# Optimization experiments

Measured on AMD Instinct MI355X. Metric: run time of the kernel, lower is better.

Reference implementation:

```python
import jax, jax.numpy as jnp
import numpy as np
import math

B, S, D, H = 4, 1024, 1024, 16
DK = D // H


def setup_inputs() -> dict:
    key = jax.random.key(0)
    ks = jax.random.split(key, 13)
    s = 1.0 / math.sqrt(D)
    inp = {
        "query": jax.random.normal(ks[0], (B, S, D), jnp.float32),
        "key": jax.random.normal(ks[1], (B, S, D), jnp.float32),
        "value": jax.random.normal(ks[2], (B, S, D), jnp.float32),
        "mask": jax.random.randint(ks[3], (B, S, S), 0, 2, jnp.int32),
        "wq": jax.random.normal(ks[4], (D, D), jnp.float32) * s,
        "bq": jax.random.normal(ks[5], (D,), jnp.float32) * s,
        "wk": jax.random.normal(ks[6], (D, D), jnp.float32) * s,
        "bk": jax.random.normal(ks[7], (D,), jnp.float32) * s,
        "wv": jax.random.normal(ks[8], (D, D), jnp.float32) * s,
        "bv": jax.random.normal(ks[9], (D,), jnp.float32) * s,
        "wo": jax.random.normal(ks[10], (D, D), jnp.float32) * s,
        "bo": jax.random.normal(ks[11], (D,), jnp.float32) * s,
    }
    return inp


def reference(query, key, value, mask, wq, bq, wk, bk, wv, bv, wo, bo):
    # QKV projections, split into heads: [B,S,D] -> [B,H,S,DK]
    def proj(x, w, b):
        return (x @ w.T + b).reshape(B, S, H, DK).transpose(0, 2, 1, 3)

    q = proj(query, wq, bq)
    k = proj(key, wk, bk)
    v = proj(value, wv, bv)

    scores = jnp.einsum("bhqd,bhkd->bhqk", q, k) / math.sqrt(DK)
    scores = scores + mask[:, None, :, :].astype(scores.dtype) * (-1e9)
    p = jax.nn.softmax(scores, axis=-1)
    x = jnp.einsum("bhqk,bhkd->bhqd", p, v)
    x = x.transpose(0, 2, 1, 3).reshape(B, S, D)
    # output projection (dropout is identity in eval)
    return x @ wo.T + bo
```

## Files before the change

### kernel.cpp

```cpp
#include <hip/hip_runtime.h>
#include <hip/hip_bf16.h>


typedef __bf16 bf16x8 __attribute__((ext_vector_type(8)));
typedef float f32x4 __attribute__((ext_vector_type(4)));
typedef unsigned short us8 __attribute__((ext_vector_type(8)));
typedef unsigned short us4 __attribute__((ext_vector_type(4)));

#define MFMA(a, b, c) __builtin_amdgcn_mfma_f32_16x16x32_bf16(a, b, c, 0, 0, 0)
#define EXP2(x) __builtin_amdgcn_exp2f(x)

__device__ __forceinline__ unsigned short f2b(float f) {
  return __builtin_bit_cast(unsigned short, __float2bfloat16(f));
}
__device__ __forceinline__ float b2f(unsigned short u) {
  return __builtin_bit_cast(float, (unsigned)u << 16);
}
__device__ __forceinline__ bf16x8 ldbf8(const unsigned short* p) {
  return __builtin_bit_cast(bf16x8, *reinterpret_cast<const us8*>(p));
}
__device__ __forceinline__ us8 cvt8(float4 a, float4 b) {
  us8 o;
  o[0] = f2b(a.x); o[1] = f2b(a.y); o[2] = f2b(a.z); o[3] = f2b(a.w);
  o[4] = f2b(b.x); o[5] = f2b(b.y); o[6] = f2b(b.z); o[7] = f2b(b.w);
  return o;
}
__device__ __forceinline__ void glds16(const void* g, void* l) {
  __builtin_amdgcn_global_load_lds(
      (const __attribute__((address_space(1))) unsigned int*)g,
      (__attribute__((address_space(3))) unsigned int*)l, 16, 0, 0);
}

__global__ __launch_bounds__(256)
void prep(const int* __restrict__ mask, const float* __restrict__ wq,
          const float* __restrict__ wk, const float* __restrict__ wv,
          unsigned short* __restrict__ Mf, unsigned short* __restrict__ Wb) {
  const int bid = blockIdx.x, tid = threadIdx.x;
  if (bid < 4096) {
    const int idx = bid * 256 + tid;
    const int wl = idx & 63, tile = idx >> 6;
    const int kt = tile & 63, qt = (tile >> 6) & 63, b = tile >> 12;
    const int lr = wl & 15, lg = wl >> 4;
    const int4 mv = *reinterpret_cast<const int4*>(
        mask + (size_t)(b * 1024 + qt * 16 + lr) * 1024 + kt * 16 + lg * 4);
    us4 o;
    o[0] = mv.x ? 0xCEACu : 0u;
    o[1] = mv.y ? 0xCEACu : 0u;
    o[2] = mv.z ? 0xCEACu : 0u;
    o[3] = mv.w ? 0xCEACu : 0u;
    *reinterpret_cast<us4*>(Mf + (size_t)idx * 4) = o;
  } else {
    const int b2 = bid - 4096;
    const int widx = b2 >> 9;
    const float* src = (widx == 0) ? wq : (widx == 1) ? wk : wv;
    const size_t off = (size_t)(b2 & 511) * 2048 + tid * 8;
    const float4* p = reinterpret_cast<const float4*>(src + off);
    *reinterpret_cast<us8*>(Wb + (size_t)widx * 1048576 + off) = cvt8(p[0], p[1]);
  }
}

__global__ __launch_bounds__(256)
void cvt_w(const float* __restrict__ src, unsigned short* __restrict__ dst) {
  const size_t off = (size_t)blockIdx.x * 2048 + threadIdx.x * 8;
  const float4* p = reinterpret_cast<const float4*>(src + off);
  *reinterpret_cast<us8*>(dst + off) = cvt8(p[0], p[1]);
}

#define GEMM_COMPUTE_HALF(buf, h2)                                             \
  {                                                                            \
    bf16x8 af[4], bfr[2];                                                      \
    _Pragma("unroll") for (int m = 0; m < 4; ++m) {                            \
      const int row = wr * 64 + m * 16 + lr;                                   \
      af[m] = ldbf8((const unsigned short*)((char*)&As[buf][0] + row * 128 +   \
                                            (((h2) * 64 + lg * 16) ^ swzc)));  \
    }                                                                          \
    _Pragma("unroll") for (int n = 0; n < 2; ++n) {                            \
      const int row = wc * 32 + n * 16 + lr;                                   \
      bfr[n] = ldbf8((const unsigned short*)((char*)&Bs[buf][0] + row * 128 +  \
                                             (((h2) * 64 + lg * 16) ^ swzc))); \
    }                                                                          \
    _Pragma("unroll") for (int m = 0; m < 4; ++m)                              \
        _Pragma("unroll") for (int n = 0; n < 2; ++n)                          \
        acc[m][n] = MFMA(af[m], bfr[n], acc[m][n]);                            \
  }

#define STA(buf, it, v)                                                        \
  *reinterpret_cast<us8*>((char*)&As[buf][0] + (srow + (it) * 32) * 128 +      \
                          (scolb ^ (((srow + (it) * 32) & 7) << 4))) = (v)

__global__ __launch_bounds__(256)
void gemm_qkv(const float* __restrict__ Aq, const float* __restrict__ Akk,
              const float* __restrict__ Av, const unsigned short* __restrict__ Wb,
              const float* __restrict__ bq, const float* __restrict__ bk,
              const float* __restrict__ bv, unsigned short* __restrict__ Qb,
              unsigned short* __restrict__ Kf, unsigned short* __restrict__ Vf,
              float qscale) {
  constexpr int K = 1024, N = 1024;
  __shared__ __align__(16) unsigned short As[2][128 * 64];
  __shared__ __align__(16) unsigned short Bs[2][64 * 64];
  const int lid = blockIdx.x + (blockIdx.y << 5) + (blockIdx.z << 9);
  const int xcd = lid & 7, slot = lid >> 3;
  const int chunk = ((slot >> 5) << 3) + xcd;
  const int pos = slot & 31;
  const int z = chunk >> 4;
  const int bm = (((chunk & 15) << 1) + (pos >> 4)) * 128;
  const int bn = (pos & 15) * 64;

  const float* A = (z == 0) ? Aq : (z == 1) ? Akk : Av;
  const unsigned short* Bw = Wb + (size_t)z * 1048576;
  const float* bias = (z == 0) ? bq : (z == 1) ? bk : bv;
  const int t = threadIdx.x;
  const int w = t >> 6, lane = t & 63, lr = lane & 15, lg = lane >> 4;
  const int wr = w >> 1, wc = w & 1;
  const int srow = t >> 3, scolb = (t & 7) * 16, scole = (t & 7) * 8;
  const int swzc = (lr & 7) << 4;

  f32x4 acc[4][2];
#pragma unroll
  for (int m = 0; m < 4; ++m)
#pragma unroll
    for (int n = 0; n < 2; ++n) acc[m][n] = f32x4{0.f, 0.f, 0.f, 0.f};

  auto stageB = [&](int k0, int buf) {
#pragma unroll
    for (int it = 0; it < 2; ++it) {
      const int s = it * 256 + t, row = s >> 3, cb = (s & 7) * 16;
      const char* g = (const char*)Bw + ((size_t)(bn + row) * 1024 + k0) * 2 +
                      (cb ^ ((row & 7) << 4));
      char* l = (char*)&Bs[buf][0] + (it * 256 + w * 64) * 16;
      glds16(g, l);
    }
  };

  {
#pragma unroll
    for (int it = 0; it < 4; ++it) {
      const float4* p =
          reinterpret_cast<const float4*>(A + (size_t)(bm + srow + it * 32) * K + scole);
      STA(0, it, cvt8(p[0], p[1]));
    }
    stageB(0, 0);
  }
  __syncthreads();

  for (int c = 0; c < 16; ++c) {
    const int buf = c & 1;
    float4 fa[8];
    if (c < 15) {
      const int k1 = (c + 1) * 64;
#pragma unroll
      for (int it = 0; it < 4; ++it) {
        const float4* p = reinterpret_cast<const float4*>(
            A + (size_t)(bm + srow + it * 32) * K + k1 + scole);
        fa[2 * it] = p[0];
        fa[2 * it + 1] = p[1];
      }
      stageB(k1, buf ^ 1);
    }
    GEMM_COMPUTE_HALF(buf, 0)
    GEMM_COMPUTE_HALF(buf, 1)
    if (c < 15) {
#pragma unroll
      for (int it = 0; it < 4; ++it) STA(buf ^ 1, it, cvt8(fa[2 * it], fa[2 * it + 1]));
    }
    __syncthreads();
  }

#pragma unroll
  for (int m = 0; m < 4; ++m) {
    const int mr = bm + wr * 64 + m * 16 + lg * 4;
#pragma unroll
    for (int nt = 0; nt < 2; ++nt) {
      const int n = bn + wc * 32 + nt * 16 + lr;
      const float bb = bias[n];
      if (z == 0) {
#pragma unroll
        for (int r = 0; r < 4; ++r)
          Qb[(size_t)(mr + r) * N + n] = f2b((acc[m][nt][r] + bb) * qscale);
      } else if (z == 1) {
        const int b2 = mr >> 10, s0 = mr & 1023, hh = n >> 6, dd = n & 63;
        const size_t base = (size_t)(b2 * 16 + hh) * 65536 + (size_t)(dd >> 5) * 32768 +
                            (size_t)(s0 >> 4) * 512 +
                            (size_t)((s0 & 15) | (((dd >> 3) & 3) << 4)) * 8 + (dd & 7);
#pragma unroll
        for (int r = 0; r < 4; ++r) Kf[base + r * 8] = f2b(acc[m][nt][r] + bb);
      } else {
        const int b2 = mr >> 10, s0 = mr & 1023, hh = n >> 6, dd = n & 63;
        const size_t base = (size_t)(b2 * 16 + hh) * 65536 + (size_t)(s0 >> 5) * 2048 +
                            (size_t)(dd >> 4) * 512 +
                            (size_t)((dd & 15) | (((s0 >> 3) & 3) << 4)) * 8 + (s0 & 7);
        us4 pk;
#pragma unroll
        for (int r = 0; r < 4; ++r) pk[r] = f2b(acc[m][nt][r] + bb);
        *reinterpret_cast<us4*>(&Vf[base]) = pk;
      }
    }
  }
}

__global__ __launch_bounds__(256)
void gemm_out(const unsigned short* __restrict__ A, const unsigned short* __restrict__ Bw,
              const float* __restrict__ bias, float* __restrict__ Out) {
  constexpr int K = 1024, N = 1024;
  __shared__ __align__(16) unsigned short As[2][128 * 64];
  __shared__ __align__(16) unsigned short Bs[2][64 * 64];
  const int lid = blockIdx.x + (blockIdx.y << 5);
  const int xcd = lid & 7, slot = lid >> 3;
  const int chunk = ((slot >> 5) << 3) + xcd;
  const int pos = slot & 31;
  const int bm = ((chunk << 1) + (pos >> 4)) * 128;
  const int bn = (pos & 15) * 64;
  const int t = threadIdx.x;
  const int w = t >> 6, lane = t & 63, lr = lane & 15, lg = lane >> 4;
  const int wr = w >> 1, wc = w & 1;
  const int swzc = (lr & 7) << 4;

  f32x4 acc[4][2];
#pragma unroll
  for (int m = 0; m < 4; ++m)
#pragma unroll
    for (int n = 0; n < 2; ++n) acc[m][n] = f32x4{0.f, 0.f, 0.f, 0.f};

  auto stageA = [&](int k0, int buf) {
#pragma unroll
    for (int it = 0; it < 4; ++it) {
      const int s = it * 256 + t, row = s >> 3, cb = (s & 7) * 16;
      const char* g = (const char*)A + ((size_t)(bm + row) * 1024 + k0) * 2 +
                      (cb ^ ((row & 7) << 4));
      char* l = (char*)&As[buf][0] + (it * 256 + w * 64) * 16;
      glds16(g, l);
    }
  };
  auto stageB = [&](int k0, int buf) {
#pragma unroll
    for (int it = 0; it < 2; ++it) {
      const int s = it * 256 + t, row = s >> 3, cb = (s & 7) * 16;
      const char* g = (const char*)Bw + ((size_t)(bn + row) * 1024 + k0) * 2 +
                      (cb ^ ((row & 7) << 4));
      char* l = (char*)&Bs[buf][0] + (it * 256 + w * 64) * 16;
      glds16(g, l);
    }
  };

  stageA(0, 0);
  stageB(0, 0);
  __syncthreads();

  for (int c = 0; c < 16; ++c) {
    const int buf = c & 1;
    if (c < 15) {
      const int k1 = (c + 1) * 64;
      stageA(k1, buf ^ 1);
      stageB(k1, buf ^ 1);
    }
    GEMM_COMPUTE_HALF(buf, 0)
    GEMM_COMPUTE_HALF(buf, 1)
    __syncthreads();
  }

#pragma unroll
  for (int m = 0; m < 4; ++m) {
    const int mr = bm + wr * 64 + m * 16 + lg * 4;
#pragma unroll
    for (int nt = 0; nt < 2; ++nt) {
      const int n = bn + wc * 32 + nt * 16 + lr;
      const float bb = bias[n];
#pragma unroll
      for (int r = 0; r < 4; ++r) Out[(size_t)(mr + r) * N + n] = acc[m][nt][r] + bb;
    }
  }
}

__global__ __launch_bounds__(256)
void attn_v5(const unsigned short* __restrict__ Qb,
             const unsigned short* __restrict__ Kf,
             const unsigned short* __restrict__ Vf,
             const unsigned short* __restrict__ Mf,
             unsigned short* __restrict__ ctx) {
  __shared__ __align__(16) unsigned short sP[4][16 * 64];
  const int lid = blockIdx.x + (blockIdx.y << 6);
  const int xcd = lid & 7, slot = lid >> 3;
  const int bh = ((slot >> 4) << 3) + xcd;
  const int qb = slot & 15;
  const int b = bh >> 4, h = bh & 15;
  const int t = threadIdx.x, w = t >> 6, wl = t & 63, lr = wl & 15, lg = wl >> 4;
  const int q0 = qb * 64 + w * 16;
  const int swz = (lr & 7) << 4;

  const unsigned short* qp = Qb + (size_t)(b * 1024 + q0 + lr) * 1024 + h * 64 + lg * 8;
  const bf16x8 bq0 = ldbf8(qp);
  const bf16x8 bq1 = ldbf8(qp + 32);

  const unsigned short* KfB = Kf + (size_t)bh * 65536;
  const unsigned short* VfB = Vf + (size_t)bh * 65536;
  const unsigned short* mfp = Mf + (size_t)((b * 64 + qb * 4 + w) * 64) * 256 + wl * 4;

  f32x4 O[4];
  float m_ = -3e38f, l_ = 0.f;
#pragma unroll
  for (int dt = 0; dt < 4; ++dt) O[dt] = f32x4{0.f, 0.f, 0.f, 0.f};
  unsigned short* sp = &sP[w][0];

  for (int kc = 0; kc < 16; ++kc) {
    bf16x8 ak[4][2];
#pragma unroll
    for (int t4 = 0; t4 < 4; ++t4) {
      ak[t4][0] = ldbf8(KfB + (size_t)(kc * 4 + t4) * 512 + wl * 8);
      ak[t4][1] = ldbf8(KfB + 32768 + (size_t)(kc * 4 + t4) * 512 + wl * 8);
    }
    us4 mk[4];
#pragma unroll
    for (int t4 = 0; t4 < 4; ++t4)
      mk[t4] = *reinterpret_cast<const us4*>(mfp + (size_t)(kc * 4 + t4) * 256);
    bf16x8 bv[2][4];
#pragma unroll
    for (int ks = 0; ks < 2; ++ks)
#pragma unroll
      for (int dt = 0; dt < 4; ++dt)
        bv[ks][dt] = ldbf8(VfB + (size_t)(kc * 2 + ks) * 2048 + dt * 512 + wl * 8);

    f32x4 sc[4];
#pragma unroll
    for (int t4 = 0; t4 < 4; ++t4) {
      f32x4 a;
#pragma unroll
      for (int r = 0; r < 4; ++r) a[r] = b2f(mk[t4][r]);
      a = MFMA(ak[t4][0], bq0, a);
      a = MFMA(ak[t4][1], bq1, a);
      sc[t4] = a;
    }

    float v0 = fmaxf(fmaxf(sc[0][0], sc[0][1]), fmaxf(sc[0][2], sc[0][3]));
    float v1 = fmaxf(fmaxf(sc[1][0], sc[1][1]), fmaxf(sc[1][2], sc[1][3]));
    float v2 = fmaxf(fmaxf(sc[2][0], sc[2][1]), fmaxf(sc[2][2], sc[2][3]));
    float v3 = fmaxf(fmaxf(sc[3][0], sc[3][1]), fmaxf(sc[3][2], sc[3][3]));
    float mc = fmaxf(fmaxf(v0, v1), fmaxf(v2, v3));
    mc = fmaxf(mc, __shfl_xor(mc, 16));
    mc = fmaxf(mc, __shfl_xor(mc, 32));
    if (__any(mc > m_ + 11.5f)) {
      const float mn = fmaxf(m_, mc);
      const float sf = EXP2(m_ - mn);
      l_ *= sf;
      m_ = mn;
      float s4[4];
#pragma unroll
      for (int r = 0; r < 4; ++r) s4[r] = __shfl(sf, lg * 4 + r);
#pragma unroll
      for (int dt = 0; dt < 4; ++dt)
#pragma unroll
        for (int r = 0; r < 4; ++r) O[dt][r] *= s4[r];
    }
    float ps = 0.f;
#pragma unroll
    for (int t4 = 0; t4 < 4; ++t4) {
      us4 pw;
#pragma unroll
      for (int r = 0; r < 4; ++r) {
        const float e = EXP2(sc[t4][r] - m_);
        ps += e;
        pw[r] = f2b(e);
      }
      *reinterpret_cast<us4*>((char*)sp + lr * 128 + ((t4 * 32 + lg * 8) ^ swz)) = pw;
    }
    ps += __shfl_xor(ps, 16);
    ps += __shfl_xor(ps, 32);
    l_ += ps;

#pragma unroll
    for (int ks = 0; ks < 2; ++ks) {
      bf16x8 ap =
          ldbf8((const unsigned short*)((char*)sp + lr * 128 + ((ks * 64 + lg * 16) ^ swz)));
#pragma unroll
      for (int dt = 0; dt < 4; ++dt) O[dt] = MFMA(ap, bv[ks][dt], O[dt]);
    }
  }

  float linv[4];
#pragma unroll
  for (int r = 0; r < 4; ++r) linv[r] = 1.0f / __shfl(l_, lg * 4 + r);
#pragma unroll
  for (int dt = 0; dt < 4; ++dt)
#pragma unroll
    for (int r = 0; r < 4; ++r)
      ctx[(size_t)(b * 1024 + q0 + lg * 4 + r) * 1024 + h * 64 + dt * 16 + lr] =
          f2b(O[dt][r] * linv[r]);
}

extern "C" void kernel_launch(void* const* d_in, const int* in_sizes, int n_in,
                              void* d_out, int out_size, void* d_ws, size_t ws_size,
                              hipStream_t stream) {
  const float* query = (const float*)d_in[0];
  const float* key   = (const float*)d_in[1];
  const float* value = (const float*)d_in[2];
  const int*   mask  = (const int*)d_in[3];
  const float* wq = (const float*)d_in[4];
  const float* bq = (const float*)d_in[5];
  const float* wk = (const float*)d_in[6];
  const float* bk = (const float*)d_in[7];
  const float* wv = (const float*)d_in[8];
  const float* bv = (const float*)d_in[9];
  const float* wo = (const float*)d_in[10];
  const float* bo = (const float*)d_in[11];
  float* out = (float*)d_out;

  const size_t SZ = (size_t)4096 * 1024;
  unsigned short* Qb  = (unsigned short*)d_ws;
  unsigned short* Kf  = Qb + SZ;
  unsigned short* Vf  = Kf + SZ;
  unsigned short* ctx = Vf + SZ;
  unsigned short* Mf  = (unsigned short*)d_out;
  unsigned short* Wb  = Mf + SZ;
  unsigned short* Wob = Vf;

  const float qscale = 0.125f * 1.4426950408889634f;
  dim3 blk(256);
  prep<<<5632, blk, 0, stream>>>(mask, wq, wk, wv, Mf, Wb);
  gemm_qkv<<<dim3(32, 16, 3), blk, 0, stream>>>(query, key, value, Wb, bq, bk, bv,
                                                Qb, Kf, Vf, qscale);
  attn_v5<<<dim3(64, 16), blk, 0, stream>>>(Qb, Kf, Vf, Mf, ctx);
  cvt_w<<<512, blk, 0, stream>>>(wo, Wob);
  gemm_out<<<dim3(32, 16), blk, 0, stream>>>(ctx, Wob, bo, out);
}
```

Baseline: 130.1 us.

## Pre-convert QKV activations to bf16 and widen projection GEMM tiles to 128x128

The prep kernel now converts the query/key/value activations to bf16 in scratch buffers, so the projection GEMM can stage A with direct global-to-LDS loads instead of loading fp32 into registers and converting. The projection GEMM tile grows from 128x64 to 128x128, giving each wave a 4x4 MFMA block for more reuse. Mask conversion moves into its own kernel launched after the GEMM, because its output buffer now overlaps the bf16 activation buffers. The change adds an extra round-trip of activations through memory and an extra launch. The fp32 value path is kept as a fallback for when the workspace is too small.

```diff
diff --git a/kernel.cpp b/kernel.cpp
--- a/kernel.cpp
+++ b/kernel.cpp
@@ -32,31 +32,45 @@
 }
 
 __global__ __launch_bounds__(256)
-void prep(const int* __restrict__ mask, const float* __restrict__ wq,
+void prep(const float* __restrict__ query, const float* __restrict__ key,
+          const float* __restrict__ value, const float* __restrict__ wq,
           const float* __restrict__ wk, const float* __restrict__ wv,
-          unsigned short* __restrict__ Mf, unsigned short* __restrict__ Wb) {
+          unsigned short* __restrict__ Abfq, unsigned short* __restrict__ Abfk,
+          unsigned short* __restrict__ Abfv, unsigned short* __restrict__ Wb) {
   const int bid = blockIdx.x, tid = threadIdx.x;
-  if (bid < 4096) {
-    const int idx = bid * 256 + tid;
-    const int wl = idx & 63, tile = idx >> 6;
-    const int kt = tile & 63, qt = (tile >> 6) & 63, b = tile >> 12;
-    const int lr = wl & 15, lg = wl >> 4;
-    const int4 mv = *reinterpret_cast<const int4*>(
-        mask + (size_t)(b * 1024 + qt * 16 + lr) * 1024 + kt * 16 + lg * 4);
-    us4 o;
-    o[0] = mv.x ? 0xCEACu : 0u;
-    o[1] = mv.y ? 0xCEACu : 0u;
-    o[2] = mv.z ? 0xCEACu : 0u;
-    o[3] = mv.w ? 0xCEACu : 0u;
-    *reinterpret_cast<us4*>(Mf + (size_t)idx * 4) = o;
+  const float* src;
+  unsigned short* dst;
+  size_t off;
+  if (bid < 1536) {
+    const int widx = bid >> 9;
+    src = (widx == 0) ? wq : (widx == 1) ? wk : wv;
+    dst = Wb + (size_t)widx * 1048576;
+    off = (size_t)(bid & 511) * 2048 + tid * 8;
+  } else if (bid < 3584) {
+    src = query; dst = Abfq; off = (size_t)(bid - 1536) * 2048 + tid * 8;
+  } else if (bid < 5632) {
+    src = key; dst = Abfk; off = (size_t)(bid - 3584) * 2048 + tid * 8;
   } else {
-    const int b2 = bid - 4096;
-    const int widx = b2 >> 9;
-    const float* src = (widx == 0) ? wq : (widx == 1) ? wk : wv;
-    const size_t off = (size_t)(b2 & 511) * 2048 + tid * 8;
-    const float4* p = reinterpret_cast<const float4*>(src + off);
-    *reinterpret_cast<us8*>(Wb + (size_t)widx * 1048576 + off) = cvt8(p[0], p[1]);
-  }
+    src = value; dst = Abfv; off = (size_t)(bid - 5632) * 2048 + tid * 8;
+  }
+  const float4* p = reinterpret_cast<const float4*>(src + off);
+  *reinterpret_cast<us8*>(dst + off) = cvt8(p[0], p[1]);
+}
+
+__global__ __launch_bounds__(256)
+void maskcvt(const int* __restrict__ mask, unsigned short* __restrict__ Mf) {
+  const int idx = blockIdx.x * 256 + threadIdx.x;
+  const int wl = idx & 63, tile = idx >> 6;
+  const int kt = tile & 63, qt = (tile >> 6) & 63, b = tile >> 12;
+  const int lr = wl & 15, lg = wl >> 4;
+  const int4 mv = *reinterpret_cast<const int4*>(
+      mask + (size_t)(b * 1024 + qt * 16 + lr) * 1024 + kt * 16 + lg * 4);
+  us4 o;
+  o[0] = mv.x ? 0xCEACu : 0u;
+  o[1] = mv.y ? 0xCEACu : 0u;
+  o[2] = mv.z ? 0xCEACu : 0u;
+  o[3] = mv.w ? 0xCEACu : 0u;
+  *reinterpret_cast<us4*>(Mf + (size_t)idx * 4) = o;
 }
 
 __global__ __launch_bounds__(256)
@@ -66,47 +80,28 @@
   *reinterpret_cast<us8*>(dst + off) = cvt8(p[0], p[1]);
 }
 
-#define GEMM_COMPUTE_HALF(buf, h2)                                             \
-  {                                                                            \
-    bf16x8 af[4], bfr[2];                                                      \
-    _Pragma("unroll") for (int m = 0; m < 4; ++m) {                            \
-      const int row = wr * 64 + m * 16 + lr;                                   \
-      af[m] = ldbf8((const unsigned short*)((char*)&As[buf][0] + row * 128 +   \
-                                            (((h2) * 64 + lg * 16) ^ swzc)));  \
-    }                                                                          \
-    _Pragma("unroll") for (int n = 0; n < 2; ++n) {                            \
-      const int row = wc * 32 + n * 16 + lr;                                   \
-      bfr[n] = ldbf8((const unsigned short*)((char*)&Bs[buf][0] + row * 128 +  \
-                                             (((h2) * 64 + lg * 16) ^ swzc))); \
-    }                                                                          \
-    _Pragma("unroll") for (int m = 0; m < 4; ++m)                              \
-        _Pragma("unroll") for (int n = 0; n < 2; ++n)                          \
-        acc[m][n] = MFMA(af[m], bfr[n], acc[m][n]);                            \
-  }
-
-#define STA(buf, it, v)                                                        \
-  *reinterpret_cast<us8*>((char*)&As[buf][0] + (srow + (it) * 32) * 128 +      \
-                          (scolb ^ (((srow + (it) * 32) & 7) << 4))) = (v)
-
-__global__ __launch_bounds__(256)
-void gemm_qkv(const float* __restrict__ Aq, const float* __restrict__ Akk,
-              const float* __restrict__ Av, const unsigned short* __restrict__ Wb,
-              const float* __restrict__ bq, const float* __restrict__ bk,
-              const float* __restrict__ bv, unsigned short* __restrict__ Qb,
-              unsigned short* __restrict__ Kf, unsigned short* __restrict__ Vf,
-              float qscale) {
+__global__ __launch_bounds__(256)
+void gemm_proj(const unsigned short* __restrict__ Aq,
+               const unsigned short* __restrict__ Ak,
+               const unsigned short* __restrict__ Av_bf,
+               const float* __restrict__ Av_f32,
+               const unsigned short* __restrict__ Wb,
+               const float* __restrict__ bq, const float* __restrict__ bk,
+               const float* __restrict__ bv, unsigned short* __restrict__ Qb,
+               unsigned short* __restrict__ Kf, unsigned short* __restrict__ Vf,
+               float qscale) {
   constexpr int K = 1024, N = 1024;
   __shared__ __align__(16) unsigned short As[2][128 * 64];
-  __shared__ __align__(16) unsigned short Bs[2][64 * 64];
-  const int lid = blockIdx.x + (blockIdx.y << 5) + (blockIdx.z << 9);
+  __shared__ __align__(16) unsigned short Bs[2][128 * 64];
+  const int lid = blockIdx.x + (blockIdx.y << 5) + (blockIdx.z << 8);
   const int xcd = lid & 7, slot = lid >> 3;
-  const int chunk = ((slot >> 5) << 3) + xcd;
-  const int pos = slot & 31;
-  const int z = chunk >> 4;
-  const int bm = (((chunk & 15) << 1) + (pos >> 4)) * 128;
-  const int bn = (pos & 15) * 64;
-
-  const float* A = (z == 0) ? Aq : (z == 1) ? Akk : Av;
+  const int chunk = ((slot >> 3) << 3) + xcd;
+  const int z = chunk >> 5;
+  const int bm = (chunk & 31) * 128;
+  const int bn = (slot & 7) * 128;
+
+  const unsigned short* Abf = (z == 0) ? Aq : (z == 1) ? Ak : Av_bf;
+  const bool f32path = (z == 2) && (Av_bf == nullptr);
   const unsigned short* Bw = Wb + (size_t)z * 1048576;
   const float* bias = (z == 0) ? bq : (z == 1) ? bk : bv;
   const int t = threadIdx.x;
@@ -115,15 +110,25 @@
   const int srow = t >> 3, scolb = (t & 7) * 16, scole = (t & 7) * 8;
   const int swzc = (lr & 7) << 4;
 
-  f32x4 acc[4][2];
+  f32x4 acc[4][4];
 #pragma unroll
   for (int m = 0; m < 4; ++m)
 #pragma unroll
-    for (int n = 0; n < 2; ++n) acc[m][n] = f32x4{0.f, 0.f, 0.f, 0.f};
-
+    for (int n = 0; n < 4; ++n) acc[m][n] = f32x4{0.f, 0.f, 0.f, 0.f};
+
+  auto stageA = [&](int k0, int buf) {
+#pragma unroll
+    for (int it = 0; it < 4; ++it) {
+      const int s = it * 256 + t, row = s >> 3, cb = (s & 7) * 16;
+      const char* g = (const char*)Abf + ((size_t)(bm + row) * 1024 + k0) * 2 +
+                      (cb ^ ((row & 7) << 4));
+      char* l = (char*)&As[buf][0] + (it * 256 + w * 64) * 16;
+      glds16(g, l);
+    }
+  };
   auto stageB = [&](int k0, int buf) {
 #pragma unroll
-    for (int it = 0; it < 2; ++it) {
+    for (int it = 0; it < 4; ++it) {
       const int s = it * 256 + t, row = s >> 3, cb = (s & 7) * 16;
       const char* g = (const char*)Bw + ((size_t)(bn + row) * 1024 + k0) * 2 +
                       (cb ^ ((row & 7) << 4));
@@ -131,16 +136,21 @@
       glds16(g, l);
     }
   };
-
-  {
+#define STA8(buf, it, v)                                                       \
+  *reinterpret_cast<us8*>((char*)&As[buf][0] + (srow + (it) * 32) * 128 +      \
+                          (scolb ^ (((srow + (it) * 32) & 7) << 4))) = (v)
+
+  if (f32path) {
 #pragma unroll
     for (int it = 0; it < 4; ++it) {
-      const float4* p =
-          reinterpret_cast<const float4*>(A + (size_t)(bm + srow + it * 32) * K + scole);
-      STA(0, it, cvt8(p[0], p[1]));
-    }
-    stageB(0, 0);
-  }
+      const float4* p = reinterpret_cast<const float4*>(
+          Av_f32 + (size_t)(bm + srow + it * 32) * K + scole);
+      STA8(0, it, cvt8(p[0], p[1]));
+    }
+  } else {
+    stageA(0, 0);
+  }
+  stageB(0, 0);
   __syncthreads();
 
   for (int c = 0; c < 16; ++c) {
@@ -148,30 +158,53 @@
     float4 fa[8];
     if (c < 15) {
       const int k1 = (c + 1) * 64;
-#pragma unroll
-      for (int it = 0; it < 4; ++it) {
-        const float4* p = reinterpret_cast<const float4*>(
-            A + (size_t)(bm + srow + it * 32) * K + k1 + scole);
-        fa[2 * it] = p[0];
-        fa[2 * it + 1] = p[1];
+      if (f32path) {
+#pragma unroll
+        for (int it = 0; it < 4; ++it) {
+          const float4* p = reinterpret_cast<const float4*>(
+              Av_f32 + (size_t)(bm + srow + it * 32) * K + k1 + scole);
+          fa[2 * it] = p[0];
+          fa[2 * it + 1] = p[1];
+        }
+      } else {
+        stageA(k1, buf ^ 1);
       }
       stageB(k1, buf ^ 1);
     }
-    GEMM_COMPUTE_HALF(buf, 0)
-    GEMM_COMPUTE_HALF(buf, 1)
-    if (c < 15) {
-#pragma unroll
-      for (int it = 0; it < 4; ++it) STA(buf ^ 1, it, cvt8(fa[2 * it], fa[2 * it + 1]));
+#pragma unroll
+    for (int h2 = 0; h2 < 2; ++h2) {
+      bf16x8 af[4], bfr[4];
+#pragma unroll
+      for (int m = 0; m < 4; ++m) {
+        const int row = wr * 64 + m * 16 + lr;
+        af[m] = ldbf8((const unsigned short*)((char*)&As[buf][0] + row * 128 +
+                                              ((h2 * 64 + lg * 16) ^ swzc)));
+      }
+#pragma unroll
+      for (int n = 0; n < 4; ++n) {
+        const int row = wc * 64 + n * 16 + lr;
+        bfr[n] = ldbf8((const unsigned short*)((char*)&Bs[buf][0] + row * 128 +
+                                               ((h2 * 64 + lg * 16) ^ swzc)));
+      }
+#pragma unroll
+      for (int m = 0; m < 4; ++m)
+#pragma unroll
+        for (int n = 0; n < 4; ++n) acc[m][n] = MFMA(af[m], bfr[n], acc[m][n]);
+    }
+    if (c < 15 && f32path) {
+#pragma unroll
+      for (int it = 0; it < 4; ++it) STA8(buf ^ 1, it, cvt8(fa[2 * it], fa[2 * it + 1]));
     }
     __syncthreads();
   }
+#undef STA8
 
 #pragma unroll
   for (int m = 0; m < 4; ++m) {
     const int mr = bm + wr * 64 + m * 16 + lg * 4;
 #pragma unroll
-    for (int nt = 0; nt < 2; ++nt) {
-      const int n = bn + wc * 32 + nt * 16 + lr;
+    for (int nt = 0; nt < 4; ++nt) {
+      const int n = bn + wc * 64 + nt * 16 + lr;
       const float bb = bias[n];
       if (z == 0) {
 #pragma unroll
@@ -253,8 +286,26 @@
       stageA(k1, buf ^ 1);
       stageB(k1, buf ^ 1);
     }
-    GEMM_COMPUTE_HALF(buf, 0)
-    GEMM_COMPUTE_HALF(buf, 1)
+#pragma unroll
+    for (int h2 = 0; h2 < 2; ++h2) {
+      bf16x8 af[4], bfr[2];
+#pragma unroll
+      for (int m = 0; m < 4; ++m) {
+        const int row = wr * 64 + m * 16 + lr;
+        af[m] = ldbf8((const unsigned short*)((char*)&As[buf][0] + row * 128 +
+                                              ((h2 * 64 + lg * 16) ^ swzc)));
+      }
+#pragma unroll
+      for (int n = 0; n < 2; ++n) {
+        const int row = wc * 32 + n * 16 + lr;
+        bfr[n] = ldbf8((const unsigned short*)((char*)&Bs[buf][0] + row * 128 +
+                                               ((h2 * 64 + lg * 16) ^ swzc)));
+      }
+#pragma unroll
+      for (int m = 0; m < 4; ++m)
+#pragma unroll
+        for (int n = 0; n < 2; ++n) acc[m][n] = MFMA(af[m], bfr[n], acc[m][n]);
+    }
     __syncthreads();
   }
 
@@ -404,19 +455,25 @@
   float* out = (float*)d_out;
 
   const size_t SZ = (size_t)4096 * 1024;
-  unsigned short* Qb  = (unsigned short*)d_ws;
-  unsigned short* Kf  = Qb + SZ;
-  unsigned short* Vf  = Kf + SZ;
-  unsigned short* ctx = Vf + SZ;
-  unsigned short* Mf  = (unsigned short*)d_out;
-  unsigned short* Wb  = Mf + SZ;
-  unsigned short* Wob = Vf;
+  unsigned short* Qb   = (unsigned short*)d_ws;
+  unsigned short* Kf   = Qb + SZ;
+  unsigned short* Vf   = Kf + SZ;
+  unsigned short* ctx  = Vf + SZ;
+  unsigned short* Abfq = (unsigned short*)d_out;
+  unsigned short* Wb   = Abfq + SZ;
+  unsigned short* Mf   = (unsigned short*)d_out;
+  unsigned short* Abfk = ctx;
+  const bool big = ws_size >= (size_t)40 * 1024 * 1024;
+  unsigned short* Abfv = big ? (ctx + SZ) : nullptr;
+  unsigned short* Wob  = Vf;
 
   const float qscale = 0.125f * 1.4426950408889634f;
   dim3 blk(256);
-  prep<<<5632, blk, 0, stream>>>(mask, wq, wk, wv, Mf, Wb);
-  gemm_qkv<<<dim3(32, 16, 3), blk, 0, stream>>>(query, key, value, Wb, bq, bk, bv,
-                                                Qb, Kf, Vf, qscale);
+  prep<<<big ? 7680 : 5632, blk, 0, stream>>>(query, key, value, wq, wk, wv,
+                                              Abfq, Abfk, Abfv, Wb);
+  gemm_proj<<<dim3(32, 8, 3), blk, 0, stream>>>(Abfq, Abfk, Abfv, value, Wb,
+                                                bq, bk, bv, Qb, Kf, Vf, qscale);
+  maskcvt<<<4096, blk, 0, stream>>>(mask, Mf);
   attn_v5<<<dim3(64, 16), blk, 0, stream>>>(Qb, Kf, Vf, Mf, ctx);
   cvt_w<<<512, blk, 0, stream>>>(wo, Wob);
   gemm_out<<<dim3(32, 16), blk, 0, stream>>>(ctx, Wob, bo, out);
```

New measurement: 130.2 us. Within noise of the previous version (+0.1%).
